# Optimization experiments

Measured on AMD Instinct MI355X. Metric: run time of the kernel, lower is better.

The kernel has to match this reference:

```python
import math
import jax, jax.numpy as jnp
import numpy as np

IN_CH = 512
OUT_CH = 512
KSIZE = 3
STYLE_DIM = 512
EPS = 1e-8


def setup_inputs() -> dict:
    key = jax.random.key(0)
    ks = jax.random.split(key, 8)
    B, H, W = 16, 32, 32
    x = jax.random.normal(ks[0], (B, IN_CH, H, W), dtype=jnp.float32)
    style = jax.random.normal(ks[1], (B, STYLE_DIM), dtype=jnp.float32)
    noise = jax.random.normal(ks[2], (B, 1, 2 * H, 2 * W), dtype=jnp.float32)
    # learned params (matching torch init semantics)
    conv_weight = jax.random.normal(ks[3], (OUT_CH, IN_CH, KSIZE, KSIZE), dtype=jnp.float32)
    mod_weight = jax.random.normal(ks[4], (IN_CH, STYLE_DIM), dtype=jnp.float32)
    mod_bias = jnp.ones((IN_CH,), dtype=jnp.float32)  # bias_init=1
    noise_weight = jax.random.normal(ks[5], (1,), dtype=jnp.float32) * 0.1
    act_bias = jnp.zeros((OUT_CH,), dtype=jnp.float32)
    return {"x": x, "style": style, "noise": noise, "conv_weight": conv_weight,
            "mod_weight": mod_weight, "mod_bias": mod_bias,
            "noise_weight": noise_weight, "act_bias": act_bias}


def _blur_kernel_2d():
    k = jnp.array([1.0, 3.0, 3.0, 1.0], dtype=jnp.float32)
    k2 = k[None, :] * k[:, None]
    k2 = k2 / k2.sum()
    return k2 * 4.0  # upsample_factor**2


def _styled_conv_up(x, style, conv_weight, mod_weight, mod_bias,
                    noise_weight, act_bias, noise):
    B, C_in, H, W = x.shape
    # EqualLinear modulation: scale = 1/sqrt(style_dim), lr_mul=1
    s = style @ (mod_weight * (1.0 / math.sqrt(STYLE_DIM))).T + mod_bias  # [B, C_in]
    # modulate + demodulate per-sample weights
    wscale = 1.0 / math.sqrt(C_in * KSIZE * KSIZE)
    w = wscale * conv_weight[None] * s[:, None, :, None, None]  # [B, out, in, k, k]
    demod = jax.lax.rsqrt(jnp.sum(w * w, axis=(2, 3, 4)) + EPS)  # [B, out]
    w = w * demod[:, :, None, None, None]
    # conv_transpose2d(stride=2, padding=0) == lhs_dilated conv with spatially
    # flipped kernel. torch passes weight as (in, out, k, k); equivalent OIHW
    # forward kernel is flip(w) with layout (out, in, k, k).
    w_flip = jnp.flip(w, axis=(-2, -1))

    def single(xi, wi):  # xi [in,H,W], wi [out,in,k,k]
        return jax.lax.conv_general_dilated(
            xi[None], wi, window_strides=(1, 1),
            padding=[(KSIZE - 1, KSIZE - 1)] * 2,
            lhs_dilation=(2, 2),
            dimension_numbers=("NCHW", "OIHW", "NCHW"))[0]

    out = jax.vmap(single)(x, w_flip)  # [B, out, 2H+1, 2W+1] for k=3
    # Blur: upfirdn2d(kernel=4x4, pad=(1,1)) -> depthwise valid conv
    Bc, Co, Ho, Wo = out.shape
    kb = _blur_kernel_2d()[None, None]  # [1,1,4,4] (symmetric, flip is a no-op)
    out = jax.lax.conv_general_dilated(
        out.reshape(Bc * Co, 1, Ho, Wo), kb, window_strides=(1, 1),
        padding=[(1, 1), (1, 1)],
        dimension_numbers=("NCHW", "OIHW", "NCHW"))
    out = out.reshape(Bc, Co, Ho + 2 - 3, Wo + 2 - 3)  # [B, out, 2H, 2W]
    # noise injection + FusedLeakyReLU (slope 0.2, scale sqrt(2))
    out = out + noise_weight * noise
    out = jax.nn.leaky_relu(out + act_bias.reshape(1, -1, 1, 1), 0.2) * math.sqrt(2.0)
    return out


def reference(x, style, noise, conv_weight, mod_weight, mod_bias,
              noise_weight, act_bias):
    return _styled_conv_up(x, style, conv_weight, mod_weight, mod_bias,
                           noise_weight, act_bias, noise)
```

## Files before the change

### kernel.cpp

```cpp
#include <hip/hip_runtime.h>
#include <math.h>


typedef __attribute__((ext_vector_type(8))) __bf16 bf16x8;
typedef __attribute__((ext_vector_type(4))) float f32x4;

#define WSCALE 0.014731391274719739f
#define SSCALE 0.044194173824159216f

__device__ __forceinline__ unsigned short f2bf(float f) {
  unsigned u = __builtin_bit_cast(unsigned, f);
  u += 0x7fff + ((u >> 16) & 1);
  return (unsigned short)(u >> 16);
}
__device__ __forceinline__ float bf2f(unsigned short h) {
  unsigned u = ((unsigned)h) << 16;
  return __builtin_bit_cast(float, u);
}

__global__ __launch_bounds__(256) void k_style(
    const float* __restrict__ style, const float* __restrict__ mod_w,
    const float* __restrict__ mod_b, float* __restrict__ s_out) {
  int wid  = (blockIdx.x * 256 + threadIdx.x) >> 6;
  int lane = threadIdx.x & 63;
  int b = wid >> 9, ic = wid & 511;
  float acc = 0.f;
  for (int j = lane; j < 512; j += 64)
    acc += style[b * 512 + j] * mod_w[ic * 512 + j];
  for (int off = 32; off > 0; off >>= 1) acc += __shfl_down(acc, off);
  if (lane == 0) s_out[b * 512 + ic] = acc * SSCALE + mod_b[ic];
}

__global__ __launch_bounds__(256) void k_w2(
    const float* __restrict__ conv_w, unsigned short* __restrict__ W2,
    float* __restrict__ w2s) {
  __shared__ float t[4608];
  const int oc = blockIdx.x;
  for (int i = threadIdx.x; i < 4608; i += 256) t[i] = conv_w[oc * 4608 + i];
  __syncthreads();
  for (int i = threadIdx.x; i < 4608; i += 256) {
    int tg = i >> 9, ic = i & 511;
    W2[((size_t)(tg * 512 + oc)) * 512 + ic] = f2bf(t[ic * 9 + tg]);
  }
  for (int i = threadIdx.x; i < 512; i += 256) {
    float a = 0.f;
    #pragma unroll
    for (int tg = 0; tg < 9; tg++) { float w = t[i * 9 + tg]; a += w * w; }
    w2s[oc * 512 + i] = a;
  }
}

__global__ __launch_bounds__(256) void k_demod(
    const float* __restrict__ w2s, const float* __restrict__ s,
    float* __restrict__ dscale) {
  int wid  = (blockIdx.x * 256 + threadIdx.x) >> 6;
  int lane = threadIdx.x & 63;
  int b = wid >> 9, oc = wid & 511;
  float acc = 0.f;
  for (int ic = lane; ic < 512; ic += 64) {
    float sv = s[b * 512 + ic];
    acc += sv * sv * w2s[oc * 512 + ic];
  }
  for (int off = 32; off > 0; off >>= 1) acc += __shfl_down(acc, off);
  if (lane == 0)
    dscale[b * 512 + oc] = WSCALE * rsqrtf(WSCALE * WSCALE * acc + 1e-8f);
}

__global__ __launch_bounds__(256) void k_xs(
    const float* __restrict__ x, const float* __restrict__ s,
    unsigned short* __restrict__ S2) {
  __shared__ float xt[64][65];
  const int b = blockIdx.z, ic0 = blockIdx.y * 64, r0 = blockIdx.x * 2;
  for (int i = threadIdx.x; i < 4096; i += 256) {
    int icL = i >> 6, pxL = i & 63;
    int gr = r0 + (pxL >> 5), gc = pxL & 31;
    xt[icL][pxL] = x[((b * 512 + ic0 + icL) * 32 + gr) * 32 + gc] * s[b * 512 + ic0 + icL];
  }
  __syncthreads();
  for (int i = threadIdx.x; i < 512; i += 256) {
    int pxL = i >> 3, icO = i & 7;
    unsigned short tmp[8];
    #pragma unroll
    for (int k = 0; k < 8; k++) tmp[k] = f2bf(xt[icO * 8 + k][pxL]);
    int gr = r0 + (pxL >> 5), gc = pxL & 31;
    *(uint4*)(&S2[((size_t)b * 1024 + gr * 32 + gc) * 512 + ic0 + icO * 8]) =
        *(const uint4*)tmp;
  }
}

__global__ __launch_bounds__(256, 2) void k_gemm(
    const unsigned short* __restrict__ S2, const unsigned short* __restrict__ W2,
    const float* __restrict__ dscale, unsigned short* __restrict__ T, int b_base) {
  __shared__ __align__(16) unsigned short As[128][64];
  __shared__ __align__(16) unsigned short Bs[256][64];

  const int mt = blockIdx.x;
  const int nt = blockIdx.y;
  const int bl = blockIdx.z, b = b_base + bl;
  const int m0 = mt * 128;
  const int tid = threadIdx.x, lane = tid & 63;
  const int wv = tid >> 6, wm = wv >> 1, wn = wv & 1;
  const int l15 = lane & 15, quad = lane >> 4;

  const unsigned short* __restrict__ Ag = W2 + (size_t)m0 * 512;
  const unsigned short* __restrict__ Bg = S2 + ((size_t)b * 1024 + nt * 256) * 512;

  f32x4 acc[4][8];
  #pragma unroll
  for (int m = 0; m < 4; m++)
    #pragma unroll
    for (int n = 0; n < 8; n++) acc[m][n] = (f32x4)0.f;

  #pragma unroll 1
  for (int ic0 = 0; ic0 < 512; ic0 += 64) {
    __syncthreads();
    #pragma unroll
    for (int it = 0; it < 4; it++) {
      int c = it * 256 + tid, r = c >> 3, kq = c & 7;
      uint4 v = *(const uint4*)(Ag + (size_t)r * 512 + ic0 + kq * 8);
      *(uint4*)(&As[r][(kq ^ (r & 7)) * 8]) = v;
    }
    #pragma unroll
    for (int it = 0; it < 8; it++) {
      int c = it * 256 + tid, r = c >> 3, kq = c & 7;
      uint4 v = *(const uint4*)(Bg + (size_t)r * 512 + ic0 + kq * 8);
      *(uint4*)(&Bs[r][(kq ^ (r & 7)) * 8]) = v;
    }
    __syncthreads();
    #pragma unroll
    for (int kk = 0; kk < 2; kk++) {
      bf16x8 af[4], bfr[8];
      #pragma unroll
      for (int m = 0; m < 4; m++) {
        int r = wm * 64 + m * 16 + l15;
        af[m] = *(const bf16x8*)(&As[r][((kk * 4 + quad) ^ (r & 7)) * 8]);
      }
      #pragma unroll
      for (int n = 0; n < 8; n++) {
        int r = wn * 128 + n * 16 + l15;
        bfr[n] = *(const bf16x8*)(&Bs[r][((kk * 4 + quad) ^ (r & 7)) * 8]);
      }
      #pragma unroll
      for (int m = 0; m < 4; m++)
        #pragma unroll
        for (int n = 0; n < 8; n++)
          acc[m][n] = __builtin_amdgcn_mfma_f32_16x16x32_bf16(af[m], bfr[n], acc[m][n], 0, 0, 0);
    }
  }

  const int t = mt >> 2, ocb = (mt & 3) * 128;
  float dsv[4][4];
  #pragma unroll
  for (int m = 0; m < 4; m++)
    #pragma unroll
    for (int r = 0; r < 4; r++)
      dsv[m][r] = dscale[b * 512 + ocb + wm * 64 + m * 16 + quad * 4 + r];
  const size_t Tbase = ((size_t)(bl * 9 + t)) * 512 * 1024;
  #pragma unroll
  for (int n = 0; n < 8; n++) {
    int px = nt * 256 + wn * 128 + n * 16 + l15;
    #pragma unroll
    for (int m = 0; m < 4; m++) {
      int oc = ocb + wm * 64 + m * 16 + quad * 4;
      #pragma unroll
      for (int r = 0; r < 4; r++)
        T[Tbase + (size_t)(oc + r) * 1024 + px] = f2bf(acc[m][n][r] * dsv[m][r]);
    }
  }
}

__global__ __launch_bounds__(256) void k_blur(
    const unsigned short* __restrict__ T, const float* __restrict__ noise,
    const float* __restrict__ noise_w, const float* __restrict__ act_b,
    float* __restrict__ out, int b_base) {
  __shared__ __align__(16) unsigned short Tm[9][1024];
  __shared__ unsigned short Ism[4][1089];
  __shared__ float V[64][67];
  const int oc = blockIdx.x, bl = blockIdx.y, b = b_base + bl;
  for (int i = threadIdx.x; i < 1152; i += 256) {
    int tg = i >> 7, w = i & 127;
    *(uint4*)(&Tm[tg][w * 8]) =
        *(const uint4*)(T + ((size_t)(bl * 9 + tg) * 512 + oc) * 1024 + w * 8);
  }
  __syncthreads();
  for (int i = threadIdx.x; i < 4356; i += 256) {
    int p = i / 1089, u = i - p * 1089;
    int uy = u / 33, ux = u - uy * 33;
    int py = p >> 1, pxp = p & 1;
    float acc = 0.f;
    int na = py ? 1 : 2, nc = pxp ? 1 : 2;
    for (int a = 0; a < na; a++) {
      int ky = py ? 1 : a * 2;
      int iy = uy - (ky == 2);
      for (int c = 0; c < nc; c++) {
        int kx = pxp ? 1 : c * 2;
        int ix = ux - (kx == 2);
        if ((unsigned)iy < 32u && (unsigned)ix < 32u)
          acc += bf2f(Tm[ky * 3 + kx][iy * 32 + ix]);
      }
    }
    Ism[p][u] = f2bf(acc);
  }
  __syncthreads();
  for (int i = threadIdx.x; i < 2112; i += 256) {
    int r = i / 66, col = i - r * 66;
    int px_ = (col >= 33), ux = col - 33 * px_;
    float v0 = (r >= 1) ? bf2f(Ism[2 + px_][(r - 1) * 33 + ux]) : 0.f;
    float a_ = bf2f(Ism[px_][r * 33 + ux]);
    float b_ = bf2f(Ism[2 + px_][r * 33 + ux]);
    float c_ = bf2f(Ism[px_][(r + 1) * 33 + ux]);
    float d_ = bf2f(Ism[2 + px_][(r + 1) * 33 + ux]);
    V[2 * r][col]     = 0.25f * v0 + 0.75f * a_ + 0.75f * b_ + 0.25f * c_;
    V[2 * r + 1][col] = 0.25f * a_ + 0.75f * b_ + 0.75f * c_ + 0.25f * d_;
  }
  __syncthreads();
  const float nw = noise_w[0], ab = act_b[oc];
  for (int i = threadIdx.x; i < 2048; i += 256) {
    int qy = i >> 5, rx = i & 31;
    float w0 = (rx >= 1) ? V[qy][33 + rx - 1] : 0.f;
    float a_ = V[qy][rx];
    float b_ = V[qy][33 + rx];
    float c_ = V[qy][rx + 1];
    float d_ = V[qy][33 + rx + 1];
    float o0 = 0.25f * w0 + 0.75f * a_ + 0.75f * b_ + 0.25f * c_;
    float o1 = 0.25f * a_ + 0.75f * b_ + 0.75f * c_ + 0.25f * d_;
    const float2 nv = *(const float2*)(noise + b * 4096 + qy * 64 + 2 * rx);
    o0 += nw * nv.x + ab;  o1 += nw * nv.y + ab;
    o0 = (o0 > 0.f ? o0 : 0.2f * o0) * 1.4142135623730951f;
    o1 = (o1 > 0.f ? o1 : 0.2f * o1) * 1.4142135623730951f;
    float2 ov = make_float2(o0, o1);
    *(float2*)(out + (((size_t)b * 512 + oc) * 64 + qy) * 64 + 2 * rx) = ov;
  }
}

extern "C" void kernel_launch(void* const* d_in, const int* in_sizes, int n_in,
                              void* d_out, int out_size, void* d_ws, size_t ws_size,
                              hipStream_t stream) {
  const float* x       = (const float*)d_in[0];
  const float* style   = (const float*)d_in[1];
  const float* noise   = (const float*)d_in[2];
  const float* conv_w  = (const float*)d_in[3];
  const float* mod_w   = (const float*)d_in[4];
  const float* mod_b   = (const float*)d_in[5];
  const float* noise_w = (const float*)d_in[6];
  const float* act_b   = (const float*)d_in[7];
  float* out = (float*)d_out;

  char* ws = (char*)d_ws;
  float*          s_ws = (float*)ws;
  float*          d_sc = (float*)(ws + 32768);
  float*          w2s  = (float*)(ws + 65536);
  unsigned short* S2   = (unsigned short*)(ws + 65536 + 1048576);
  unsigned short* W2   = (unsigned short*)(ws + 65536 + 1048576 + 16777216);
  unsigned short* T    = (unsigned short*)(ws + 65536 + 1048576 + 16777216 + 4718592);
  const size_t fixed  = 65536ull + 1048576ull + 16777216ull + 4718592ull;
  const size_t t_full = (size_t)16 * 9 * 512 * 1024 * 2;

  int nb = 16;
  if (ws_size < fixed + t_full)     nb = 8;
  if (ws_size < fixed + t_full / 2) nb = 4;
  if (ws_size < fixed + t_full / 4) nb = 2;
  if (ws_size < fixed + t_full / 8) nb = 1;

  k_style<<<2048, 256, 0, stream>>>(style, mod_w, mod_b, s_ws);
  k_w2<<<512, 256, 0, stream>>>(conv_w, W2, w2s);
  k_demod<<<2048, 256, 0, stream>>>(w2s, s_ws, d_sc);
  k_xs<<<dim3(16, 8, 16), 256, 0, stream>>>(x, s_ws, S2);
  for (int b0 = 0; b0 < 16; b0 += nb) {
    k_gemm<<<dim3(36, 4, nb), 256, 0, stream>>>(S2, W2, d_sc, T, b0);
    k_blur<<<dim3(512, nb), 256, 0, stream>>>(T, noise, noise_w, act_b, out, b0);
  }
}
```

Measured before the change: 402.7 us.

## Fold transposed-conv tap scatter into GEMM via polyphase implicit-GEMM over padded input

Replaces the per-tap GEMM that wrote nine full tap outputs followed by a scatter-add in the blur kernel. The new GEMM computes the four stride-2 output phases directly as an implicit GEMM. The K dimension concatenates the contributing taps, reading shifted rows of a zero-padded 34x34 input buffer. This cuts the intermediate tensor from nine to four planes per channel and removes the scatter pass from the blur kernel, at the cost of per-row index computation, an extra zero-border kernel and uneven K lengths across phases (4/2/2/1 taps).

Result: slower. 483.5 us (+20.1%).

```diff
diff --git a/kernel.cpp b/kernel.cpp
--- a/kernel.cpp
+++ b/kernel.cpp
@@ -31,6 +31,11 @@
   if (lane == 0) s_out[b * 512 + ic] = acc * SSCALE + mod_b[ic];
 }
 
+__device__ const int SLABTAP[9] = {0, 2, 6, 8, 1, 7, 3, 5, 4};
+__device__ const int SLABOFF[4] = {0, 4, 6, 8};
+__device__ const int TAPN[4]    = {4, 2, 2, 1};
+__device__ const int TOFFp[4][4] = {{0,-1,-34,-35},{0,-34,0,0},{0,-1,0,0},{0,0,0,0}};
+
 __global__ __launch_bounds__(256) void k_w2(
     const float* __restrict__ conv_w, unsigned short* __restrict__ W2,
     float* __restrict__ w2s) {
@@ -40,7 +45,7 @@
   __syncthreads();
   for (int i = threadIdx.x; i < 4608; i += 256) {
     int tg = i >> 9, ic = i & 511;
-    W2[((size_t)(tg * 512 + oc)) * 512 + ic] = f2bf(t[ic * 9 + tg]);
+    W2[((size_t)(tg * 512 + oc)) * 512 + ic] = f2bf(t[ic * 9 + SLABTAP[tg]]);
   }
   for (int i = threadIdx.x; i < 512; i += 256) {
     float a = 0.f;
@@ -66,7 +71,7 @@
     dscale[b * 512 + oc] = WSCALE * rsqrtf(WSCALE * WSCALE * acc + 1e-8f);
 }
 
-__global__ __launch_bounds__(256) void k_xs(
+__global__ __launch_bounds__(256) void k_xs2(
     const float* __restrict__ x, const float* __restrict__ s,
     unsigned short* __restrict__ S2) {
   __shared__ float xt[64][65];
@@ -83,27 +88,50 @@
     #pragma unroll
     for (int k = 0; k < 8; k++) tmp[k] = f2bf(xt[icO * 8 + k][pxL]);
     int gr = r0 + (pxL >> 5), gc = pxL & 31;
-    *(uint4*)(&S2[((size_t)b * 1024 + gr * 32 + gc) * 512 + ic0 + icO * 8]) =
-        *(const uint4*)tmp;
-  }
+    int R = (gr + 1) * 34 + (gc + 1);
+    *(uint4*)(&S2[((size_t)b * 1156 + R) * 512 + ic0 + icO * 8]) = *(const uint4*)tmp;
+  }
+}
+
+__global__ void k_zero(unsigned short* __restrict__ S2) {
+  int b = blockIdx.y, id = blockIdx.x;
+  int ry, rx;
+  if (id < 34)       { ry = 0;        rx = id; }
+  else if (id < 68)  { ry = 33;       rx = id - 34; }
+  else if (id < 100) { ry = id - 67;  rx = 0; }
+  else               { ry = id - 99;  rx = 33; }
+  ((unsigned*)(S2 + ((size_t)b * 1156 + ry * 34 + rx) * 512))[threadIdx.x] = 0;
 }
 
 __global__ __launch_bounds__(256, 2) void k_gemm(
     const unsigned short* __restrict__ S2, const unsigned short* __restrict__ W2,
-    const float* __restrict__ dscale, unsigned short* __restrict__ T, int b_base) {
+    const float* __restrict__ dscale, unsigned short* __restrict__ I,
+    int b_base, int nTot) {
   __shared__ __align__(16) unsigned short As[128][64];
   __shared__ __align__(16) unsigned short Bs[256][64];
 
   const int mt = blockIdx.x;
   const int nt = blockIdx.y;
-  const int bl = blockIdx.z, b = b_base + bl;
-  const int m0 = mt * 128;
+  const int p  = blockIdx.z;
+  const int m0 = mt * 128, n0 = nt * 256;
   const int tid = threadIdx.x, lane = tid & 63;
   const int wv = tid >> 6, wm = wv >> 1, wn = wv & 1;
   const int l15 = lane & 15, quad = lane >> 4;
-
-  const unsigned short* __restrict__ Ag = W2 + (size_t)m0 * 512;
-  const unsigned short* __restrict__ Bg = S2 + ((size_t)b * 1024 + nt * 256) * 512;
+  const int ntap = TAPN[p], soff = SLABOFF[p];
+  const int kq = tid & 7;
+
+  int gRow[8];
+  #pragma unroll
+  for (int it = 0; it < 8; it++) {
+    int r = it * 32 + (tid >> 3);
+    int n = n0 + r;
+    if (n < nTot) {
+      int bl = n / 1089;
+      int u = n - bl * 1089;
+      int uy = u / 33, ux = u - uy * 33;
+      gRow[it] = (b_base + bl) * 1156 + (uy + 1) * 34 + (ux + 1);
+    } else gRow[it] = -1;
+  }
 
   f32x4 acc[4][8];
   #pragma unroll
@@ -111,19 +139,26 @@
     #pragma unroll
     for (int n = 0; n < 8; n++) acc[m][n] = (f32x4)0.f;
 
+  const int kend = ntap * 512;
   #pragma unroll 1
-  for (int ic0 = 0; ic0 < 512; ic0 += 64) {
+  for (int k0 = 0; k0 < kend; k0 += 64) {
+    const int tj   = k0 >> 9;
+    const int icw  = k0 & 511;
+    const int off  = TOFFp[p][tj];
+    const int slab = soff + tj;
     __syncthreads();
     #pragma unroll
     for (int it = 0; it < 4; it++) {
-      int c = it * 256 + tid, r = c >> 3, kq = c & 7;
-      uint4 v = *(const uint4*)(Ag + (size_t)r * 512 + ic0 + kq * 8);
+      int r = it * 32 + (tid >> 3);
+      uint4 v = *(const uint4*)(W2 + ((size_t)(slab * 512 + m0 + r)) * 512 + icw + kq * 8);
       *(uint4*)(&As[r][(kq ^ (r & 7)) * 8]) = v;
     }
     #pragma unroll
     for (int it = 0; it < 8; it++) {
-      int c = it * 256 + tid, r = c >> 3, kq = c & 7;
-      uint4 v = *(const uint4*)(Bg + (size_t)r * 512 + ic0 + kq * 8);
+      int r = it * 32 + (tid >> 3);
+      uint4 v = make_uint4(0u, 0u, 0u, 0u);
+      if (gRow[it] >= 0)
+        v = *(const uint4*)(S2 + (size_t)(gRow[it] + off) * 512 + icw + kq * 8);
       *(uint4*)(&Bs[r][(kq ^ (r & 7)) * 8]) = v;
     }
     __syncthreads();
@@ -148,58 +183,37 @@
     }
   }
 
-  const int t = mt >> 2, ocb = (mt & 3) * 128;
-  float dsv[4][4];
-  #pragma unroll
-  for (int m = 0; m < 4; m++)
-    #pragma unroll
-    for (int r = 0; r < 4; r++)
-      dsv[m][r] = dscale[b * 512 + ocb + wm * 64 + m * 16 + quad * 4 + r];
-  const size_t Tbase = ((size_t)(bl * 9 + t)) * 512 * 1024;
   #pragma unroll
   for (int n = 0; n < 8; n++) {
-    int px = nt * 256 + wn * 128 + n * 16 + l15;
-    #pragma unroll
-    for (int m = 0; m < 4; m++) {
-      int oc = ocb + wm * 64 + m * 16 + quad * 4;
-      #pragma unroll
-      for (int r = 0; r < 4; r++)
-        T[Tbase + (size_t)(oc + r) * 1024 + px] = f2bf(acc[m][n][r] * dsv[m][r]);
+    int nf = n0 + wn * 128 + n * 16 + l15;
+    if (nf < nTot) {
+      int bl = nf / 1089;
+      int ul = nf - bl * 1089;
+      const size_t Ibase = ((size_t)(bl * 4 + p) * 512) * 1096;
+      #pragma unroll
+      for (int m = 0; m < 4; m++) {
+        int oc = m0 + wm * 64 + m * 16 + quad * 4;
+        #pragma unroll
+        for (int r = 0; r < 4; r++) {
+          float ds = dscale[(b_base + bl) * 512 + oc + r];
+          I[Ibase + (size_t)(oc + r) * 1096 + ul] = f2bf(acc[m][n][r] * ds);
+        }
+      }
     }
   }
 }
 
 __global__ __launch_bounds__(256) void k_blur(
-    const unsigned short* __restrict__ T, const float* __restrict__ noise,
+    const unsigned short* __restrict__ I, const float* __restrict__ noise,
     const float* __restrict__ noise_w, const float* __restrict__ act_b,
     float* __restrict__ out, int b_base) {
-  __shared__ __align__(16) unsigned short Tm[9][1024];
-  __shared__ unsigned short Ism[4][1089];
+  __shared__ __align__(16) unsigned short Ism[4][1096];
   __shared__ float V[64][67];
   const int oc = blockIdx.x, bl = blockIdx.y, b = b_base + bl;
-  for (int i = threadIdx.x; i < 1152; i += 256) {
-    int tg = i >> 7, w = i & 127;
-    *(uint4*)(&Tm[tg][w * 8]) =
-        *(const uint4*)(T + ((size_t)(bl * 9 + tg) * 512 + oc) * 1024 + w * 8);
-  }
-  __syncthreads();
-  for (int i = threadIdx.x; i < 4356; i += 256) {
-    int p = i / 1089, u = i - p * 1089;
-    int uy = u / 33, ux = u - uy * 33;
-    int py = p >> 1, pxp = p & 1;
-    float acc = 0.f;
-    int na = py ? 1 : 2, nc = pxp ? 1 : 2;
-    for (int a = 0; a < na; a++) {
-      int ky = py ? 1 : a * 2;
-      int iy = uy - (ky == 2);
-      for (int c = 0; c < nc; c++) {
-        int kx = pxp ? 1 : c * 2;
-        int ix = ux - (kx == 2);
-        if ((unsigned)iy < 32u && (unsigned)ix < 32u)
-          acc += bf2f(Tm[ky * 3 + kx][iy * 32 + ix]);
-      }
-    }
-    Ism[p][u] = f2bf(acc);
+  for (int i = threadIdx.x; i < 548; i += 256) {
+    int p = i / 137, w = i - p * 137;
+    *(uint4*)(&Ism[p][w * 8]) =
+        *(const uint4*)(I + ((size_t)(bl * 4 + p) * 512 + oc) * 1096 + w * 8);
   }
   __syncthreads();
   for (int i = threadIdx.x; i < 2112; i += 256) {
@@ -251,23 +265,25 @@
   float*          d_sc = (float*)(ws + 32768);
   float*          w2s  = (float*)(ws + 65536);
   unsigned short* S2   = (unsigned short*)(ws + 65536 + 1048576);
-  unsigned short* W2   = (unsigned short*)(ws + 65536 + 1048576 + 16777216);
-  unsigned short* T    = (unsigned short*)(ws + 65536 + 1048576 + 16777216 + 4718592);
-  const size_t fixed  = 65536ull + 1048576ull + 16777216ull + 4718592ull;
-  const size_t t_full = (size_t)16 * 9 * 512 * 1024 * 2;
+  unsigned short* W2   = (unsigned short*)(ws + 65536 + 1048576 + 18939904);
+  unsigned short* I    = (unsigned short*)(ws + 65536 + 1048576 + 18939904 + 4718592);
+  const size_t fixed = 65536ull + 1048576ull + 18939904ull + 4718592ull;
+  const size_t per_b = (size_t)4 * 512 * 1096 * 2;
 
   int nb = 16;
-  if (ws_size < fixed + t_full)     nb = 8;
-  if (ws_size < fixed + t_full / 2) nb = 4;
-  if (ws_size < fixed + t_full / 4) nb = 2;
-  if (ws_size < fixed + t_full / 8) nb = 1;
+  if (ws_size < fixed + 16 * per_b) nb = 8;
+  if (ws_size < fixed + 8 * per_b)  nb = 4;
+  if (ws_size < fixed + 4 * per_b)  nb = 2;
+  if (ws_size < fixed + 2 * per_b)  nb = 1;
 
   k_style<<<2048, 256, 0, stream>>>(style, mod_w, mod_b, s_ws);
   k_w2<<<512, 256, 0, stream>>>(conv_w, W2, w2s);
   k_demod<<<2048, 256, 0, stream>>>(w2s, s_ws, d_sc);
-  k_xs<<<dim3(16, 8, 16), 256, 0, stream>>>(x, s_ws, S2);
+  k_xs2<<<dim3(16, 8, 16), 256, 0, stream>>>(x, s_ws, S2);
+  k_zero<<<dim3(132, 16), 256, 0, stream>>>(S2);
   for (int b0 = 0; b0 < 16; b0 += nb) {
-    k_gemm<<<dim3(36, 4, nb), 256, 0, stream>>>(S2, W2, d_sc, T, b0);
-    k_blur<<<dim3(512, nb), 256, 0, stream>>>(T, noise, noise_w, act_b, out, b0);
-  }
-}
+    int nTot = nb * 1089;
+    k_gemm<<<dim3(4, (nTot + 255) / 256, 4), 256, 0, stream>>>(S2, W2, d_sc, I, b0, nTot);
+    k_blur<<<dim3(512, nb), 256, 0, stream>>>(I, noise, noise_w, act_b, out, b0);
+  }
+}
```
